# Kernel optimization log

Hardware: AMD Instinct MI355X
Metric: run time of the kernel (lower is better)

## Reference

```python
import jax, jax.numpy as jnp
import numpy as np

B, T, D = 4, 8192, 512
H, BS = 8, 16


def setup_inputs() -> dict:
    key = jax.random.key(0)
    ks = jax.random.split(key, 7)
    s = 1.0 / np.sqrt(D)
    return {
        "x": jax.random.normal(ks[0], (B, T, D), dtype=jnp.float32),
        "Wq": jax.random.normal(ks[1], (D, D), dtype=jnp.float32) * s,
        "bq": jax.random.normal(ks[2], (D,), dtype=jnp.float32) * 0.02,
        "Wk": jax.random.normal(ks[3], (D, D), dtype=jnp.float32) * s,
        "bk": jax.random.normal(ks[4], (D,), dtype=jnp.float32) * 0.02,
        "Wv": jax.random.normal(ks[5], (D, D), dtype=jnp.float32) * s,
        "bv": jax.random.normal(ks[6], (D,), dtype=jnp.float32) * 0.02,
    }


def reference(x, Wq, bq, Wk, bk, Wv, bv):
    b, t, d_model = x.shape
    nb = t // BS          # number of blocks
    dh = d_model // H     # per-head dim
    # [B,T,D] -> [B,nb,BS,D] -> [B,BS,nb,D]: attention runs across blocks
    xb = x.reshape(b, nb, BS, d_model).transpose(0, 2, 1, 3)
    # projections (torch Linear: x @ W.T + b)
    q = xb @ Wq.T + bq
    k = xb @ Wk.T + bk
    v = xb @ Wv.T + bv
    # split heads: [B,BS,nb,H,dh] -> [B,BS,H,nb,dh]
    q = q.reshape(b, BS, nb, H, dh).transpose(0, 1, 3, 2, 4)
    k = k.reshape(b, BS, nb, H, dh).transpose(0, 1, 3, 2, 4)
    v = v.reshape(b, BS, nb, H, dh).transpose(0, 1, 3, 2, 4)
    scale = d_model ** (-0.5)  # note: full dim, as in the original
    attn = jnp.einsum('bshnd,bshmd->bshnm', q, k) * scale  # [B,BS,H,nb,nb]
    attn = jax.nn.softmax(attn, axis=-1)
    out = jnp.einsum('bshnm,bshmd->bshnd', attn, v)        # [B,BS,H,nb,dh]
    # merge heads and undo block permute
    out = out.transpose(0, 1, 3, 2, 4).reshape(b, BS, nb, d_model)
    out = out.transpose(0, 2, 1, 3).reshape(b, t, d_model)
    return out
```

## Files before the change

### kernel.cpp

```cpp
#include <hip/hip_runtime.h>
#include <hip/hip_bf16.h>
#include <cstdint>
#include <cstddef>

#define Bsz 4
#define Tsz 8192
#define Dsz 512
#define Hn 8
#define BSn 16
#define NBn 512
#define DHn 64
#define NQKV 1536
#define MROWS 32768

#define SCL 0.06375870136f
#define ATT_M 8.0f

typedef __attribute__((ext_vector_type(8))) short short8;
typedef __attribute__((ext_vector_type(4))) float float4f;

__device__ __forceinline__ uint16_t f2b(float f) {
  union { float f; uint32_t u; } v; v.f = f;
  uint32_t u = v.u;
  return (uint16_t)((u + 0x7fffu + ((u >> 16) & 1u)) >> 16);
}

__device__ __forceinline__ uint32_t pk2(float a, float b) {
  union { float f; uint32_t u; } x, y; x.f = a; y.f = b;
  return __builtin_amdgcn_perm(y.u + 0x8000u, x.u + 0x8000u, 0x07060302u);
}

__device__ __forceinline__ uint32_t pk2t(float a, float b) {
  union { float f; uint32_t u; } x, y; x.f = a; y.f = b;
  return __builtin_amdgcn_perm(y.u, x.u, 0x07060302u);
}

__device__ __forceinline__ void gl_lds16(const void* g, void* l) {
  __builtin_amdgcn_global_load_lds(
      (const __attribute__((address_space(1))) unsigned int*)g,
      (__attribute__((address_space(3))) unsigned int*)l, 16, 0, 0);
}

#define XBLK (MROWS * Dsz / 1024)
__global__ void cvt_kernel(const float* __restrict__ x, const float* __restrict__ Wq,
                           const float* __restrict__ Wk, const float* __restrict__ Wv,
                           uint16_t* __restrict__ xb, uint16_t* __restrict__ wc) {
  int bid = blockIdx.x;
  if (bid < XBLK) {
    int i = (bid * 256 + threadIdx.x) * 4;
    float4 v = *(const float4*)(x + i);
    uint64_t o = (uint64_t)pk2(v.x, v.y) | ((uint64_t)pk2(v.z, v.w) << 32);
    *(uint64_t*)(xb + i) = o;
  } else {
    int i = ((bid - XBLK) * 256 + threadIdx.x) * 4;
    int row = i >> 9;
    int col = i & 511;
    const float* src = (row < 512) ? Wq : ((row < 1024) ? Wk : Wv);
    float4 v = *(const float4*)(src + (size_t)(row & 511) * 512 + col);
    uint64_t o = (uint64_t)pk2(v.x, v.y) | ((uint64_t)pk2(v.z, v.w) << 32);
    *(uint64_t*)(wc + i) = o;
  }
}

#define BM 128
#define BN 64
#define BK 64

__global__ __launch_bounds__(256, 6) void gemm_qkv(
    const uint16_t* __restrict__ Xb, const uint16_t* __restrict__ Wc,
    const float* __restrict__ bq, const float* __restrict__ bkp,
    const float* __restrict__ bv, uint16_t* __restrict__ Qp,
    uint16_t* __restrict__ Kp, uint16_t* __restrict__ Vtmp) {
  __shared__ uint16_t As[BM * BK];
  __shared__ uint16_t Bs[BN * BK];
  const int tid = threadIdx.x;
  const int wave = tid >> 6, lane = tid & 63;
  const int lrow = lane & 15, quad = lane >> 4;

  int g = blockIdx.x;
  int xcd = g & 7, ii = g >> 3;
  int mt = xcd * 32 + ii / 24;
  int nt = ii - (ii / 24) * 24;
  const int m0 = mt * BM;
  const int n0 = nt * BN;
  const int wm = (wave >> 1) * 64, wn = (wave & 1) * 32;

  float4f acc[4][2] = {};

  for (int k0 = 0; k0 < Dsz; k0 += BK) {
    __syncthreads();
#pragma unroll
    for (int p = 0; p < 4; ++p) {
      int cbase = p * 256 + wave * 64;
      int c = cbase + lane;
      int row = c >> 3, pos = c & 7;
      int kc = (pos ^ (row & 7)) * 8;
      gl_lds16(Xb + (size_t)(m0 + row) * Dsz + k0 + kc, As + cbase * 8);
    }
#pragma unroll
    for (int p = 0; p < 2; ++p) {
      int cbase = p * 256 + wave * 64;
      int c = cbase + lane;
      int row = c >> 3, pos = c & 7;
      int kc = (pos ^ (row & 7)) * 8;
      gl_lds16(Wc + (size_t)(n0 + row) * Dsz + k0 + kc, Bs + cbase * 8);
    }
    __syncthreads();

#pragma unroll
    for (int h = 0; h < 2; ++h) {
      short8 af[4], bf[2];
#pragma unroll
      for (int i = 0; i < 4; ++i) {
        int rowA = wm + i * 16 + lrow;
        af[i] = *(const short8*)(As + rowA * BK + (((h * 4 + quad) ^ (rowA & 7)) * 8));
      }
#pragma unroll
      for (int j = 0; j < 2; ++j) {
        int rowB = wn + j * 16 + lrow;
        bf[j] = *(const short8*)(Bs + rowB * BK + (((h * 4 + quad) ^ (rowB & 7)) * 8));
      }
#pragma unroll
      for (int i = 0; i < 4; ++i)
#pragma unroll
        for (int j = 0; j < 2; ++j)
          acc[i][j] = __builtin_amdgcn_mfma_f32_16x16x32_bf16(af[i], bf[j], acc[i][j], 0, 0, 0);
    }
  }

  const int region = n0 >> 9;
  const float* bias = (region == 0) ? bq : ((region == 1) ? bkp : bv);
  const float mult = (region == 0) ? SCL : 1.0f;
  const int bb = m0 >> 13;
  const int nbbase = ((m0 & 8191) >> 4) + (wm >> 4);
  const int nv0 = (n0 & 511) + wn;

  if (region < 2) {
    uint16_t* dst = (region == 0) ? Qp : Kp;
#pragma unroll
    for (int j = 0; j < 2; ++j) {
      int nl = nv0 + j * 16 + lrow;
      int hh = nl >> 6, dh = nl & 63;
      float bval = bias[nl];
      size_t base = (size_t)bb * 4194304 + (size_t)hh * 32768 +
                    (size_t)nbbase * 64 + dh + (size_t)(quad * 4) * 262144;
#pragma unroll
      for (int i = 0; i < 4; ++i)
#pragma unroll
        for (int r = 0; r < 4; ++r)
          dst[base + (size_t)r * 262144 + (size_t)i * 64] =
              f2b((acc[i][j][r] + bval) * mult);
    }
  } else {
#pragma unroll
    for (int j = 0; j < 2; ++j) {
      int nl = nv0 + j * 16 + lrow;
      float bval = bias[nl];
#pragma unroll
      for (int i = 0; i < 4; ++i) {
        int tok = m0 + wm + i * 16 + quad * 4;
#pragma unroll
        for (int r = 0; r < 4; ++r)
          Vtmp[(size_t)(tok + r) * 512 + nl] = f2b(acc[i][j][r] + bval);
      }
    }
  }
}

__global__ __launch_bounds__(256) void vtrans(const uint16_t* __restrict__ Vtmp,
                                              uint16_t* __restrict__ Vt) {
  __shared__ uint16_t tile[64 * 64];
  int bx = blockIdx.x;
  const int nt = bx & 7; bx >>= 3;
  const int h = bx & 7; bx >>= 3;
  const int s = bx & 15;
  const int b = bx >> 4;
  const int tid = threadIdx.x;

  {
    int i = tid >> 2;
    int token = b * Tsz + (nt * 64 + i) * BSn + s;
    const uint16_t* src = Vtmp + (size_t)token * 512 + h * 64;
#pragma unroll
    for (int hh = 0; hh < 2; ++hh) {
      int ch = (tid & 3) * 2 + hh;
      short8 v = *(const short8*)(src + ch * 8);
      int pc = ch ^ (i & 7);
      *(short8*)(tile + i * 64 + pc * 8) = v;
    }
  }
  __syncthreads();
  {
    int dh = tid & 63, seg = tid >> 6;
    short8 v1, v2;
#pragma unroll
    for (int k = 0; k < 8; ++k) {
      int nb_l = seg * 16 + k;
      v1[k] = (short)tile[nb_l * 64 + (((dh >> 3) ^ (nb_l & 7)) * 8) + (dh & 7)];
    }
#pragma unroll
    for (int k = 0; k < 8; ++k) {
      int nb_l = seg * 16 + 8 + k;
      v2[k] = (short)tile[nb_l * 64 + (((dh >> 3) ^ (nb_l & 7)) * 8) + (dh & 7)];
    }
    size_t obase = ((((size_t)b * 16 + s) * 8 + h) * 64 + dh) * 512 + nt * 64 + seg * 16;
    *(short8*)(Vt + obase) = v1;
    *(short8*)(Vt + obase + 8) = v2;
  }
}

__global__ __launch_bounds__(256, 3) void attn_kernel(
    const uint16_t* __restrict__ Qp, const uint16_t* __restrict__ Kp,
    const uint16_t* __restrict__ Vt, float* __restrict__ out) {
  __shared__ uint16_t Ks[32 * 64];
  __shared__ uint16_t Vs[64 * 32];
  __shared__ uint16_t Ps[4][4][16 * 32];

  int bx = blockIdx.x;
  const int qh = bx & 1; bx >>= 1;
  const int h = bx & 7; bx >>= 3;
  const int s = bx & 15;
  const int b = bx >> 4;

  const int tid = threadIdx.x;
  const int w = tid >> 6, lane = tid & 63;
  const int lrow = lane & 15, quad = lane >> 4;

  const size_t sh = (((size_t)b * 16 + s) * 8 + h);
  const uint16_t* Qb = Qp + (sh << 15);
  const uint16_t* Kb = Kp + (sh << 15);
  const uint16_t* Vb = Vt + (sh << 15);

  short8 qB[4][2];
  const int q0 = qh * 256 + w * 64;
#pragma unroll
  for (int qs = 0; qs < 4; ++qs) {
    const uint16_t* qp = Qb + (size_t)(q0 + qs * 16 + lrow) * 64;
    qB[qs][0] = *(const short8*)(qp + quad * 8);
    qB[qs][1] = *(const short8*)(qp + 32 + quad * 8);
  }

  float4f O[4][4] = {};
  float l_acc[4] = {0.f, 0.f, 0.f, 0.f};

  const int kr = w * 8 + (lane >> 3);
  const int kcs = (lane & 7) ^ (kr & 7);
  const int vr = w * 16 + (lane >> 2);
  const int vcs = (lane & 3) ^ ((vr >> 1) & 3);

  const int sw = (lrow >> 1) & 3;
  const float4f negm = {-ATT_M, -ATT_M, -ATT_M, -ATT_M};

  for (int kv0 = 0; kv0 < NBn; kv0 += 32) {
    __syncthreads();
    gl_lds16(Kb + (size_t)(kv0 + kr) * 64 + kcs * 8, Ks + w * 512);
    gl_lds16(Vb + (size_t)vr * 512 + kv0 + vcs * 8, Vs + w * 512);
    __syncthreads();

    {
      short8 kA[2][2];
#pragma unroll
      for (int kt = 0; kt < 2; ++kt) {
        int row = kt * 16 + lrow;
#pragma unroll
        for (int kc = 0; kc < 2; ++kc) {
          int cc = (kc * 4 + quad) ^ (row & 7);
          kA[kt][kc] = *(const short8*)(Ks + row * 64 + cc * 8);
        }
      }
#pragma unroll
      for (int qs = 0; qs < 4; ++qs) {
        float4f c0 = negm, c1 = negm;
        c0 = __builtin_amdgcn_mfma_f32_16x16x32_bf16(kA[0][0], qB[qs][0], c0, 0, 0, 0);
        c0 = __builtin_amdgcn_mfma_f32_16x16x32_bf16(kA[0][1], qB[qs][1], c0, 0, 0, 0);
        c1 = __builtin_amdgcn_mfma_f32_16x16x32_bf16(kA[1][0], qB[qs][0], c1, 0, 0, 0);
        c1 = __builtin_amdgcn_mfma_f32_16x16x32_bf16(kA[1][1], qB[qs][1], c1, 0, 0, 0);

        float p00 = __builtin_amdgcn_exp2f(c0[0]);
        float p01 = __builtin_amdgcn_exp2f(c0[1]);
        float p02 = __builtin_amdgcn_exp2f(c0[2]);
        float p03 = __builtin_amdgcn_exp2f(c0[3]);
        float p10 = __builtin_amdgcn_exp2f(c1[0]);
        float p11 = __builtin_amdgcn_exp2f(c1[1]);
        float p12 = __builtin_amdgcn_exp2f(c1[2]);
        float p13 = __builtin_amdgcn_exp2f(c1[3]);
        l_acc[qs] += ((p00 + p01) + (p02 + p03)) + ((p10 + p11) + (p12 + p13));

        uint32_t d0 = pk2t(p00, p01), d1 = pk2t(p02, p03);
        uint32_t d2 = pk2t(p10, p11), d3 = pk2t(p12, p13);
        uint16_t* Psq = Ps[w][qs];
        int half = (quad & 1) * 4;
        *(uint2*)(Psq + lrow * 32 + (((quad >> 1)) ^ sw) * 8 + half) = make_uint2(d0, d1);
        *(uint2*)(Psq + lrow * 32 + ((2 + (quad >> 1)) ^ sw) * 8 + half) = make_uint2(d2, d3);
      }
    }

    {
      short8 vA[4];
#pragma unroll
      for (int dt = 0; dt < 4; ++dt) {
        int row = dt * 16 + lrow;
        vA[dt] = *(const short8*)(Vs + row * 32 + (quad ^ ((row >> 1) & 3)) * 8);
      }
#pragma unroll
      for (int qs = 0; qs < 4; ++qs) {
        short8 pB = *(const short8*)(Ps[w][qs] + lrow * 32 + (quad ^ sw) * 8);
#pragma unroll
        for (int dt = 0; dt < 4; ++dt)
          O[dt][qs] = __builtin_amdgcn_mfma_f32_16x16x32_bf16(vA[dt], pB, O[dt][qs], 0, 0, 0);
      }
    }
  }

#pragma unroll
  for (int qs = 0; qs < 4; ++qs) {
    float l = l_acc[qs];
    l += __shfl_xor(l, 16);
    l += __shfl_xor(l, 32);
    float inv = 1.0f / l;
    int qg = q0 + qs * 16 + lrow;
    float* op = out + ((size_t)b * Tsz + (size_t)qg * 16 + s) * Dsz + h * 64;
#pragma unroll
    for (int dt = 0; dt < 4; ++dt) {
      float4 vv;
      vv.x = O[dt][qs][0] * inv; vv.y = O[dt][qs][1] * inv;
      vv.z = O[dt][qs][2] * inv; vv.w = O[dt][qs][3] * inv;
      *(float4*)(op + dt * 16 + quad * 4) = vv;
    }
  }
}

extern "C" void kernel_launch(void* const* d_in, const int* in_sizes, int n_in,
                              void* d_out, int out_size, void* d_ws, size_t ws_size,
                              hipStream_t stream) {
  const float* x  = (const float*)d_in[0];
  const float* Wq = (const float*)d_in[1];
  const float* bq = (const float*)d_in[2];
  const float* Wk = (const float*)d_in[3];
  const float* bk = (const float*)d_in[4];
  const float* Wv = (const float*)d_in[5];
  const float* bv = (const float*)d_in[6];
  float* out = (float*)d_out;

  uint16_t* Qp   = (uint16_t*)d_ws;
  uint16_t* Kp   = Qp + (size_t)16777216;
  uint16_t* Vtmp = Kp + (size_t)16777216;
  uint16_t* xb   = Vtmp + (size_t)16777216;
  uint16_t* wc   = xb + (size_t)16777216;
  uint16_t* Vt   = xb;

  hipLaunchKernelGGL(cvt_kernel, dim3(XBLK + NQKV * Dsz / 1024), dim3(256), 0, stream,
                     x, Wq, Wk, Wv, xb, wc);
  hipLaunchKernelGGL(gemm_qkv, dim3((MROWS / BM) * (NQKV / BN)), dim3(256), 0, stream,
                     xb, wc, bq, bk, bv, Qp, Kp, Vtmp);
  hipLaunchKernelGGL(vtrans, dim3(Bsz * BSn * Hn * 8), dim3(256), 0, stream, Vtmp, Vt);
  hipLaunchKernelGGL(attn_kernel, dim3(Bsz * BSn * Hn * 2), dim3(256), 0, stream,
                     Qp, Kp, Vt, out);
}
```

Baseline: 263.7 us.

## Rewrite QKV GEMM as 256x256 double-buffered ping-pong pipeline with 8 waves

The QKV projection GEMM moves from 128x64 tiles with single-buffered LDS and 4 waves to 256x256 tiles, 512 threads, and double-buffered LDS. Global-to-LDS staging for the next K tile is interleaved with MFMA phases, using explicit barriers, vmcnt waits and s_setprio scheduling. The goal is to hide load latency and raise arithmetic intensity per tile. In exchange it uses more LDS and registers per block, which lowers occupancy, and the grid shrinks to 768 blocks, which may hurt load balance.

```diff
diff --git a/kernel.cpp b/kernel.cpp
--- a/kernel.cpp
+++ b/kernel.cpp
@@ -62,109 +62,182 @@
   }
 }
 
-#define BM 128
-#define BN 64
+#define BM 256
+#define BN 256
 #define BK 64
 
-__global__ __launch_bounds__(256, 6) void gemm_qkv(
+__global__ __launch_bounds__(512, 2) void gemm_qkv(
     const uint16_t* __restrict__ Xb, const uint16_t* __restrict__ Wc,
     const float* __restrict__ bq, const float* __restrict__ bkp,
     const float* __restrict__ bv, uint16_t* __restrict__ Qp,
     uint16_t* __restrict__ Kp, uint16_t* __restrict__ Vtmp) {
-  __shared__ uint16_t As[BM * BK];
-  __shared__ uint16_t Bs[BN * BK];
+  __shared__ uint16_t As[2][BM * BK];
+  __shared__ uint16_t Bs[2][BN * BK];
   const int tid = threadIdx.x;
-  const int wave = tid >> 6, lane = tid & 63;
+  const int w = tid >> 6, lane = tid & 63;
   const int lrow = lane & 15, quad = lane >> 4;
+  const int wm = (w >> 2) * 128, wn = (w & 3) * 64;
 
   int g = blockIdx.x;
   int xcd = g & 7, ii = g >> 3;
-  int mt = xcd * 32 + ii / 24;
-  int nt = ii - (ii / 24) * 24;
+  int mt = xcd * 16 + ii / 6;
+  int nt = ii - (ii / 6) * 6;
   const int m0 = mt * BM;
   const int n0 = nt * BN;
-  const int wm = (wave >> 1) * 64, wn = (wave & 1) * 32;
-
-  float4f acc[4][2] = {};
-
-  for (int k0 = 0; k0 < Dsz; k0 += BK) {
-    __syncthreads();
-#pragma unroll
-    for (int p = 0; p < 4; ++p) {
-      int cbase = p * 256 + wave * 64;
-      int c = cbase + lane;
-      int row = c >> 3, pos = c & 7;
-      int kc = (pos ^ (row & 7)) * 8;
-      gl_lds16(Xb + (size_t)(m0 + row) * Dsz + k0 + kc, As + cbase * 8);
-    }
-#pragma unroll
-    for (int p = 0; p < 2; ++p) {
-      int cbase = p * 256 + wave * 64;
-      int c = cbase + lane;
-      int row = c >> 3, pos = c & 7;
-      int kc = (pos ^ (row & 7)) * 8;
-      gl_lds16(Wc + (size_t)(n0 + row) * Dsz + k0 + kc, Bs + cbase * 8);
-    }
-    __syncthreads();
-
-#pragma unroll
-    for (int h = 0; h < 2; ++h) {
-      short8 af[4], bf[2];
-#pragma unroll
-      for (int i = 0; i < 4; ++i) {
-        int rowA = wm + i * 16 + lrow;
-        af[i] = *(const short8*)(As + rowA * BK + (((h * 4 + quad) ^ (rowA & 7)) * 8));
-      }
-#pragma unroll
-      for (int j = 0; j < 2; ++j) {
-        int rowB = wn + j * 16 + lrow;
-        bf[j] = *(const short8*)(Bs + rowB * BK + (((h * 4 + quad) ^ (rowB & 7)) * 8));
-      }
-#pragma unroll
-      for (int i = 0; i < 4; ++i)
-#pragma unroll
-        for (int j = 0; j < 2; ++j)
-          acc[i][j] = __builtin_amdgcn_mfma_f32_16x16x32_bf16(af[i], bf[j], acc[i][j], 0, 0, 0);
-    }
+
+  const int r6 = tid >> 3;
+  const int kc = ((tid & 7) ^ (r6 & 7)) * 8;
+  const uint16_t* gA = Xb + (size_t)(m0 + r6) * 512 + kc;
+  const int rbB = ((r6 >> 5) * 64) + (r6 & 31);
+  const uint16_t* gB = Wc + (size_t)(n0 + rbB) * 512 + kc;
+  const int lbA = (w * 8) * 64;
+  const int lbB = ((w >> 2) * 64 + (w & 3) * 8) * 64;
+
+#define STAGE_A(buf, tile, half) do {                                         \
+    const int k0_ = (tile) * 64;                                              \
+    gl_lds16(gA + (size_t)((half) * 64) * 512 + k0_,                          \
+             &As[buf][((half) * 64) * 64 + lbA]);                             \
+    gl_lds16(gA + (size_t)((half) * 64 + 128) * 512 + k0_,                    \
+             &As[buf][((half) * 64 + 128) * 64 + lbA]);                       \
+  } while (0)
+
+#define STAGE_B(buf, tile, half) do {                                         \
+    const int k0_ = (tile) * 64;                                              \
+    gl_lds16(gB + (size_t)((half) * 32) * 512 + k0_,                          \
+             &Bs[buf][((half) * 32) * 64 + lbB]);                             \
+    gl_lds16(gB + (size_t)((half) * 32 + 128) * 512 + k0_,                    \
+             &Bs[buf][((half) * 32 + 128) * 64 + lbB]);                       \
+  } while (0)
+
+  short8 a[4][2], b0[2][2], b1[2][2];
+  float4f acc[2][2][4][2] = {};
+
+#define LOAD_A(buf, qm) do {                                                  \
+    _Pragma("unroll") for (int i_ = 0; i_ < 4; ++i_) {                        \
+      const uint16_t* p_ = &As[buf][(wm + (qm) * 64 + i_ * 16 + lrow) * 64];  \
+      a[i_][0] = *(const short8*)(p_ + ((quad ^ (lrow & 7)) * 8));            \
+      a[i_][1] = *(const short8*)(p_ + (((4 + quad) ^ (lrow & 7)) * 8));      \
+    } } while (0)
+
+#define LOAD_B(buf, qn, bb_) do {                                             \
+    _Pragma("unroll") for (int j_ = 0; j_ < 2; ++j_) {                        \
+      const uint16_t* p_ = &Bs[buf][(wn + (qn) * 32 + j_ * 16 + lrow) * 64];  \
+      bb_[j_][0] = *(const short8*)(p_ + ((quad ^ (lrow & 7)) * 8));          \
+      bb_[j_][1] = *(const short8*)(p_ + (((4 + quad) ^ (lrow & 7)) * 8));    \
+    } } while (0)
+
+#define MFMA16(QM, QN, BB) do {                                               \
+    _Pragma("unroll") for (int h_ = 0; h_ < 2; ++h_)                          \
+    _Pragma("unroll") for (int i_ = 0; i_ < 4; ++i_)                          \
+    _Pragma("unroll") for (int j_ = 0; j_ < 2; ++j_)                          \
+      acc[QM][QN][i_][j_] = __builtin_amdgcn_mfma_f32_16x16x32_bf16(          \
+          a[i_][h_], BB[j_][h_], acc[QM][QN][i_][j_], 0, 0, 0);               \
+  } while (0)
+
+#define PH_MID() do { __builtin_amdgcn_sched_barrier(0);                      \
+    __builtin_amdgcn_s_barrier(); __builtin_amdgcn_s_setprio(1); } while (0)
+#define PH_END() do { __builtin_amdgcn_s_setprio(0);                          \
+    __builtin_amdgcn_sched_barrier(0); __builtin_amdgcn_s_barrier();          \
+    __builtin_amdgcn_sched_barrier(0); } while (0)
+#define PH_END_VMC(N) do { __builtin_amdgcn_s_setprio(0);                     \
+    __builtin_amdgcn_sched_barrier(0);                                        \
+    asm volatile("s_waitcnt vmcnt(" #N ")" ::: "memory");                     \
+    __builtin_amdgcn_s_barrier();                                             \
+    __builtin_amdgcn_sched_barrier(0); } while (0)
+
+  STAGE_A(0, 0, 0); STAGE_A(0, 0, 1); STAGE_B(0, 0, 0); STAGE_B(0, 0, 1);
+  STAGE_A(1, 1, 0); STAGE_B(1, 1, 0); STAGE_B(1, 1, 1);
+  asm volatile("s_waitcnt vmcnt(6)" ::: "memory");
+  __builtin_amdgcn_s_barrier();
+  __builtin_amdgcn_sched_barrier(0);
+
+#pragma unroll 1
+  for (int it = 0; it < 4; ++it) {
+    const int t1 = 2 * it + 1;
+    const bool more = (it < 3);
+    LOAD_A(0, 0); LOAD_B(0, 0, b0);
+    STAGE_A(1, t1, 1);
+    PH_MID(); MFMA16(0, 0, b0); PH_END();
+    LOAD_B(0, 1, b1);
+    if (more) STAGE_A(0, t1 + 1, 0);
+    PH_MID(); MFMA16(0, 1, b1); PH_END();
+    LOAD_A(0, 1);
+    if (more) STAGE_B(0, t1 + 1, 0);
+    PH_MID(); MFMA16(1, 1, b1); PH_END();
+    if (more) STAGE_B(0, t1 + 1, 1);
+    PH_MID(); MFMA16(1, 0, b0);
+    if (more) PH_END_VMC(6); else PH_END_VMC(0);
+    LOAD_A(1, 0); LOAD_B(1, 0, b0);
+    if (more) STAGE_A(0, t1 + 1, 1);
+    PH_MID(); MFMA16(0, 0, b0); PH_END();
+    LOAD_B(1, 1, b1);
+    if (more) STAGE_A(1, t1 + 2, 0);
+    PH_MID(); MFMA16(0, 1, b1); PH_END();
+    LOAD_A(1, 1);
+    if (more) STAGE_B(1, t1 + 2, 0);
+    PH_MID(); MFMA16(1, 1, b1); PH_END();
+    if (more) STAGE_B(1, t1 + 2, 1);
+    PH_MID(); MFMA16(1, 0, b0);
+    if (more) PH_END_VMC(6); else PH_END();
   }
 
   const int region = n0 >> 9;
   const float* bias = (region == 0) ? bq : ((region == 1) ? bkp : bv);
-  const float mult = (region == 0) ? SCL : 1.0f;
-  const int bb = m0 >> 13;
-  const int nbbase = ((m0 & 8191) >> 4) + (wm >> 4);
-  const int nv0 = (n0 & 511) + wn;
 
   if (region < 2) {
     uint16_t* dst = (region == 0) ? Qp : Kp;
-#pragma unroll
-    for (int j = 0; j < 2; ++j) {
-      int nl = nv0 + j * 16 + lrow;
-      int hh = nl >> 6, dh = nl & 63;
-      float bval = bias[nl];
-      size_t base = (size_t)bb * 4194304 + (size_t)hh * 32768 +
-                    (size_t)nbbase * 64 + dh + (size_t)(quad * 4) * 262144;
-#pragma unroll
-      for (int i = 0; i < 4; ++i)
-#pragma unroll
-        for (int r = 0; r < 4; ++r)
-          dst[base + (size_t)r * 262144 + (size_t)i * 64] =
-              f2b((acc[i][j][r] + bval) * mult);
+    const float mult = (region == 0) ? SCL : 1.0f;
+#pragma unroll
+    for (int qm = 0; qm < 2; ++qm) {
+      const int tokb = m0 + wm + qm * 64;
+      const int bb = tokb >> 13;
+      const int nbb = (tokb >> 4) & 511;
+      const size_t base0 = (size_t)bb * 4194304 + (size_t)nbb * 64 +
+                           (size_t)(quad * 4) * 262144;
+#pragma unroll
+      for (int qn = 0; qn < 2; ++qn)
+#pragma unroll
+        for (int j = 0; j < 2; ++j) {
+          const int nl = (n0 & 511) + wn + qn * 32 + j * 16 + lrow;
+          const int hh = nl >> 6, dh = nl & 63;
+          const float bval = bias[nl];
+          const size_t base = base0 + (size_t)hh * 32768 + dh;
+#pragma unroll
+          for (int i2 = 0; i2 < 4; ++i2)
+#pragma unroll
+            for (int r = 0; r < 4; ++r)
+              dst[base + (size_t)r * 262144 + (size_t)i2 * 64] =
+                  f2b((acc[qm][qn][i2][j][r] + bval) * mult);
+        }
     }
   } else {
 #pragma unroll
-    for (int j = 0; j < 2; ++j) {
-      int nl = nv0 + j * 16 + lrow;
-      float bval = bias[nl];
-#pragma unroll
-      for (int i = 0; i < 4; ++i) {
-        int tok = m0 + wm + i * 16 + quad * 4;
-#pragma unroll
-        for (int r = 0; r < 4; ++r)
-          Vtmp[(size_t)(tok + r) * 512 + nl] = f2b(acc[i][j][r] + bval);
-      }
-    }
-  }
+    for (int qm = 0; qm < 2; ++qm) {
+      const int tokb = m0 + wm + qm * 64 + quad * 4;
+#pragma unroll
+      for (int qn = 0; qn < 2; ++qn)
+#pragma unroll
+        for (int j = 0; j < 2; ++j) {
+          const int nl = (n0 & 511) + wn + qn * 32 + j * 16 + lrow;
+          const float bval = bias[nl];
+#pragma unroll
+          for (int i2 = 0; i2 < 4; ++i2) {
+            const int tok = tokb + i2 * 16;
+#pragma unroll
+            for (int r = 0; r < 4; ++r)
+              Vtmp[(size_t)(tok + r) * 512 + nl] = f2b(acc[qm][qn][i2][j][r] + bval);
+          }
+        }
+    }
+  }
+#undef STAGE_A
+#undef STAGE_B
+#undef LOAD_A
+#undef LOAD_B
+#undef MFMA16
+#undef PH_MID
+#undef PH_END
+#undef PH_END_VMC
 }
 
 __global__ __launch_bounds__(256) void vtrans(const uint16_t* __restrict__ Vtmp,
@@ -351,7 +424,7 @@
 
   hipLaunchKernelGGL(cvt_kernel, dim3(XBLK + NQKV * Dsz / 1024), dim3(256), 0, stream,
                      x, Wq, Wk, Wv, xb, wc);
-  hipLaunchKernelGGL(gemm_qkv, dim3((MROWS / BM) * (NQKV / BN)), dim3(256), 0, stream,
+  hipLaunchKernelGGL(gemm_qkv, dim3((MROWS / BM) * (NQKV / BN)), dim3(512), 0, stream,
                      xb, wc, bq, bk, bv, Qp, Kp, Vtmp);
   hipLaunchKernelGGL(vtrans, dim3(Bsz * BSn * Hn * 8), dim3(256), 0, stream, Vtmp, Vt);
   hipLaunchKernelGGL(attn_kernel, dim3(Bsz * BSn * Hn * 2), dim3(256), 0, stream,
```

New measurement: 258.5 us. No clear change (-2.0%).
